# Optimization experiments

Hardware: AMD Instinct MI355X
Metric: run time of the kernel (lower is better)

## Reference

```python
import jax, jax.numpy as jnp
import numpy as np

B, A, N = 8, 512, 64           # structures, atoms, neighbors
D, F, G = 128, 128, 25         # atom basis, filters, gaussians
L = 3                          # interaction blocks
GA = 512                       # angular feature dim = 2*n_zetas*2*n_angular*n_zetas
MAXZ = 100
CUTOFF, START = 5.0, 1.2
LN2 = 0.6931471805599453


def ssp(x):
    # shifted softplus: ln(1+exp(x)) - ln(2)
    return jax.nn.softplus(x) - LN2


def setup_inputs() -> dict:
    key = jax.random.key(0)
    ks = jax.random.split(key, 16)
    atomic_numbers = jax.random.randint(ks[0], (B, A), 0, MAXZ, dtype=jnp.int32)
    positions = jax.random.normal(ks[1], (B, A, 3), dtype=jnp.float32) * 3.0
    neighbors = jax.random.randint(ks[2], (B, A, N), 0, A, dtype=jnp.int32)
    neighbor_mask = jax.random.randint(ks[3], (B, A, N), 0, 2, dtype=jnp.int32)
    G_i = jax.random.normal(ks[4], (B, A, GA), dtype=jnp.float32)
    s = 0.05
    embedding = jax.random.normal(ks[5], (MAXZ, D), dtype=jnp.float32) * 0.1
    embedding = embedding.at[0].set(0.0)  # padding_idx=0
    inp = {
        'atomic_numbers': atomic_numbers,
        'positions': positions,
        'neighbors': neighbors,
        'neighbor_mask': neighbor_mask,
        'G_i': G_i,
        'embedding': embedding,
        'filt_w1': jax.random.normal(ks[6], (L, G, F), dtype=jnp.float32) * s,
        'filt_b1': jnp.zeros((L, F), jnp.float32),
        'filt_w2': jax.random.normal(ks[7], (L, F, F), dtype=jnp.float32) * s,
        'filt_b2': jnp.zeros((L, F), jnp.float32),
        'in2f_w': jax.random.normal(ks[8], (L, D, F), dtype=jnp.float32) * s,
        'f2out_w': jax.random.normal(ks[9], (L, F, D), dtype=jnp.float32) * s,
        'f2out_b': jnp.zeros((L, D), jnp.float32),
        'dense_w': jax.random.normal(ks[10], (L, D, D), dtype=jnp.float32) * s,
        'dense_b': jnp.zeros((L, D), jnp.float32),
        'ang_w': jax.random.normal(ks[11], (L, GA, D), dtype=jnp.float32) * s,
    }
    return inp


def reference(atomic_numbers, positions, neighbors, neighbor_mask, G_i,
              embedding, filt_w1, filt_b1, filt_w2, filt_b2,
              in2f_w, f2out_w, f2out_b, dense_w, dense_b, ang_w):
    gather = jax.vmap(lambda feat, idx: feat[idx])  # per-structure neighbor gather

    x = embedding[atomic_numbers]                    # [B,A,D]

    # AtomDistances: gather neighbor positions and take pairwise norms
    pos_j = gather(positions, neighbors)             # [B,A,N,3]
    dvec = pos_j - positions[:, :, None, :]
    r_ij = jnp.sqrt(jnp.sum(dvec * dvec, axis=-1) + 1e-12)  # [B,A,N]

    # GaussianSmearing(start, cutoff, n_gaussians)
    offsets = jnp.linspace(START, CUTOFF, G).astype(x.dtype)
    width = offsets[1] - offsets[0]
    f_ij = jnp.exp((-0.5 / (width * width)) * (r_ij[..., None] - offsets) ** 2)  # [B,A,N,G]

    C = (r_ij <= CUTOFF).astype(x.dtype)             # HardCutoff [B,A,N]
    mask = neighbor_mask.astype(x.dtype)             # [B,A,N]

    for l in range(in2f_w.shape[0]):
        # filter-generating network on expanded distances, modulated by cutoff
        W = ssp(f_ij @ filt_w1[l] + filt_b1[l]) @ filt_w2[l] + filt_b2[l]  # [B,A,N,F]
        W = W * C[..., None]
        # CFConv: project, gather neighbors, filter-weight, masked neighbor sum
        y = x @ in2f_w[l]                            # [B,A,F]
        y_j = gather(y, neighbors)                   # [B,A,N,F]
        agg = jnp.sum(y_j * W * mask[..., None], axis=2)  # [B,A,F]
        v_rad = agg @ f2out_w[l] + f2out_b[l]        # f2out (activation=None)
        v_rad = v_rad @ dense_w[l] + dense_b[l]      # self.dense
        v_ang = G_i @ ang_w[l]                       # dense_angular (no bias)
        x = x + ssp(v_rad + v_ang)                   # residual interaction update
    return x
```

## Files before the change

kernel.cpp:

```cpp
#include <hip/hip_runtime.h>
#include <math.h>

#define NB 8
#define NA 512
#define NN 64
#define ND 128
#define NF 128
#define NG 25
#define NGA 512
#define TABN 1024

typedef __attribute__((ext_vector_type(8))) short bf16x8;
typedef __attribute__((ext_vector_type(4))) float f32x4;

__device__ __forceinline__ float sspf(float v) {
  return fmaxf(v, 0.0f) + __logf(1.0f + __expf(-fabsf(v))) - 0.6931471805599453f;
}

__device__ __forceinline__ short f2bf(float x) {
  union { float f; unsigned u; } v; v.f = x;
  unsigned r = v.u + 0x7fffu + ((v.u >> 16) & 1u);
  return (short)(r >> 16);
}

#if defined(__has_builtin)
#if __has_builtin(__builtin_amdgcn_cvt_pk_bf16_f32)
#define HAS_PKBF 1
#endif
#endif

__device__ __forceinline__ unsigned pk2bf(float a, float b) {
#ifdef HAS_PKBF
  typedef __attribute__((ext_vector_type(2))) __bf16 v2bf;
  union { v2bf v; unsigned u; } c;
  c.v = __builtin_amdgcn_cvt_pk_bf16_f32(a, b);
  return c.u;
#else
  union { float f; unsigned u; } x, y; x.f = a; y.f = b;
  const unsigned ra = (x.u + 0x7fffu + ((x.u >> 16) & 1u)) >> 16;
  const unsigned rb = (y.u + 0x7fffu + ((y.u >> 16) & 1u)) & 0xffff0000u;
  return ra | rb;
#endif
}

__device__ __forceinline__ float bf2f(unsigned short us) {
  union { unsigned u; float f; } v; v.u = ((unsigned)us) << 16; return v.f;
}

__device__ __forceinline__ bf16x8 pack8(float4 a, float4 b) {
  bf16x8 r;
  unsigned* p = (unsigned*)&r;
  p[0] = pk2bf(a.x, a.y); p[1] = pk2bf(a.z, a.w);
  p[2] = pk2bf(b.x, b.y); p[3] = pk2bf(b.z, b.w);
  return r;
}

__device__ __forceinline__ bf16x8 fragT(const float* __restrict__ M, int ldn,
                                        int n, int k0q) {
  float e[8];
#pragma unroll
  for (int i = 0; i < 8; ++i) e[i] = M[(size_t)(k0q + i) * ldn + n];
  bf16x8 r; unsigned* p = (unsigned*)&r;
  p[0] = pk2bf(e[0], e[1]); p[1] = pk2bf(e[2], e[3]);
  p[2] = pk2bf(e[4], e[5]); p[3] = pk2bf(e[6], e[7]);
  return r;
}

#define NW1 (3 * 128 * 32)
#define NSQ (3 * 128 * 128)
#define NAWT (3 * 128 * 512)

#define P1_TT 96
#define P1_AT (P1_TT + 192)
#define P1_W1 (P1_AT + 48)
#define P1_PF (P1_W1 + 24)
#define P1_TOT (P1_PF + 1024)

#define P2_VA 768
#define P2_Y0 (P2_VA + 256)
#define P2_TOT (P2_Y0 + 192)

__global__ __launch_bounds__(256) void k_prep1(
    const float* __restrict__ fw1, const float* __restrict__ fw2,
    const float* __restrict__ in2f, const float* __restrict__ aw,
    const float* __restrict__ f2o, const float* __restrict__ f2ob,
    const float* __restrict__ dw, const float* __restrict__ db,
    const float* __restrict__ Gi,
    short* __restrict__ w1T, short* __restrict__ w2T,
    short* __restrict__ in2fT, short* __restrict__ W12T,
    float* __restrict__ b12, short* __restrict__ awT,
    short* __restrict__ GiB) {
  __shared__ alignas(16) short sTile[32][33];
  const int bx = blockIdx.x;
  const int t = threadIdx.x;
  const int lane = t & 63, wave = t >> 6;
  const int lanelo = lane & 15, quad = lane >> 4;
  const int wbase = wave << 5;

  if (bx < P1_TT) {
    const int mat = bx >> 4, tile = bx & 15;
    const int l = mat >> 1, which = mat & 1;
    const float* src = (which ? in2f : fw2) + (size_t)l * 16384;
    short* dst = (which ? in2fT : w2T) + (size_t)l * 16384;
    const int tk0 = (tile >> 2) << 5, tn0 = (tile & 3) << 5;
    const int tr = t >> 3, tc4 = (t & 7) << 2;
    const float4 v = *(const float4*)(src + (size_t)(tk0 + tr) * 128 + tn0 + tc4);
    sTile[tr][tc4] = f2bf(v.x); sTile[tr][tc4 + 1] = f2bf(v.y);
    sTile[tr][tc4 + 2] = f2bf(v.z); sTile[tr][tc4 + 3] = f2bf(v.w);
    __syncthreads();
    short o[4];
#pragma unroll
    for (int j = 0; j < 4; ++j) o[j] = sTile[tc4 + j][tr];
    uint2 pk;
    pk.x = ((unsigned)(unsigned short)o[0]) | (((unsigned)(unsigned short)o[1]) << 16);
    pk.y = ((unsigned)(unsigned short)o[2]) | (((unsigned)(unsigned short)o[3]) << 16);
    *(uint2*)(dst + (size_t)(tn0 + tr) * 128 + tk0 + tc4) = pk;
    return;
  }
  if (bx < P1_AT) {
    const int ab = bx - P1_TT;
    const int l = ab >> 6, tile = ab & 63;
    const int tk0 = (tile >> 2) << 5, tn0 = (tile & 3) << 5;
    const float* src = aw + (size_t)l * 65536;
    short* dst = awT + (size_t)l * 65536;
    const int tr = t >> 3, tc4 = (t & 7) << 2;
    const float4 v = *(const float4*)(src + (size_t)(tk0 + tr) * 128 + tn0 + tc4);
    sTile[tr][tc4] = f2bf(v.x); sTile[tr][tc4 + 1] = f2bf(v.y);
    sTile[tr][tc4 + 2] = f2bf(v.z); sTile[tr][tc4 + 3] = f2bf(v.w);
    __syncthreads();
    short o[4];
#pragma unroll
    for (int j = 0; j < 4; ++j) o[j] = sTile[tc4 + j][tr];
    uint2 pk;
    pk.x = ((unsigned)(unsigned short)o[0]) | (((unsigned)(unsigned short)o[1]) << 16);
    pk.y = ((unsigned)(unsigned short)o[2]) | (((unsigned)(unsigned short)o[3]) << 16);
    *(uint2*)(dst + (size_t)(tn0 + tr) * 512 + tk0 + tc4) = pk;
    return;
  }
  if (bx < P1_W1) {
    const int idx = (bx - P1_AT) * 256 + t;
    const int l = idx >> 12, r = idx & 4095, n = r >> 5, k = r & 31;
    w1T[idx] = (k < NG) ? f2bf(fw1[(size_t)l * NG * NF + k * NF + n]) : (short)0;
    return;
  }
  if (bx < P1_PF) {
    const int fb = bx - P1_W1;
    const int l = fb >> 3, xi = fb & 7;
    const int i = (xi << 4) + lanelo;
    const float* f2o_l = f2o + (size_t)l * 16384;
    const float* dw_l = dw + (size_t)l * 16384;
    short* W12T_l = W12T + (size_t)l * 16384;
    f32x4 c[2] = {{0.f, 0.f, 0.f, 0.f}, {0.f, 0.f, 0.f, 0.f}};
#pragma unroll
    for (int kt = 0; kt < 4; ++kt) {
      const int k0 = kt * 32 + quad * 8;
      const bf16x8 b = pack8(*(const float4*)(f2o_l + (size_t)i * 128 + k0),
                             *(const float4*)(f2o_l + (size_t)i * 128 + k0 + 4));
#pragma unroll
      for (int ct = 0; ct < 2; ++ct) {
        const bf16x8 a = fragT(dw_l, 128, wbase + ct * 16 + lanelo, k0);
        c[ct] = __builtin_amdgcn_mfma_f32_16x16x32_bf16(a, b, c[ct], 0, 0, 0);
      }
    }
#pragma unroll
    for (int ct = 0; ct < 2; ++ct)
#pragma unroll
      for (int reg = 0; reg < 4; ++reg) {
        const int j = wbase + ct * 16 + quad * 4 + reg;
        W12T_l[(size_t)j * 128 + i] = f2bf(c[ct][reg]);
      }
    if (xi == 0 && t < 128) {
      float acc = db[(size_t)l * 128 + t];
      for (int k = 0; k < 128; ++k)
        acc += f2ob[(size_t)l * 128 + k] * dw_l[(size_t)k * 128 + t];
      b12[(size_t)l * 128 + t] = acc;
    }
    return;
  }
  {
    const int idx = ((bx - P1_PF) << 8) + t;
    const float* g = Gi + (size_t)idx * 8;
    const bf16x8 v = pack8(*(const float4*)g, *(const float4*)(g + 4));
    *(bf16x8*)(GiB + (size_t)idx * 8) = v;
  }
}

#define SHPAD 136
__global__ __launch_bounds__(256) void k_prep2(
    const float* __restrict__ emb, const int* __restrict__ zn,
    const short* __restrict__ GiB, const short* __restrict__ awT,
    const short* __restrict__ in2fT,
    const short* __restrict__ w1T, const short* __restrict__ w2T,
    const float* __restrict__ fb1, const float* __restrict__ fb2,
    short* __restrict__ vangB, float* __restrict__ x, short* __restrict__ yB,
    float* __restrict__ Ttab) {
  __shared__ alignas(16) short sH[16 * SHPAD];
  const int bx = blockIdx.x;
  const int t = threadIdx.x;
  const int lane = t & 63, wave = t >> 6;
  const int lanelo = lane & 15, quad = lane >> 4;
  const int wbase = wave << 5;

  if (bx < P2_VA) {
    const int l = bx >> 8;
    const int row = ((bx & 255) << 4) + lanelo;
    const short* awT_l = awT + (size_t)l * 65536;
    f32x4 c[2] = {{0.f, 0.f, 0.f, 0.f}, {0.f, 0.f, 0.f, 0.f}};
#pragma unroll
    for (int kt = 0; kt < 16; ++kt) {
      const int k0 = kt * 32 + quad * 8;
      const bf16x8 b = *(const bf16x8*)(GiB + (size_t)row * NGA + k0);
#pragma unroll
      for (int ct = 0; ct < 2; ++ct) {
        const bf16x8 a = *(const bf16x8*)(awT_l + (size_t)(wbase + ct * 16 + lanelo) * 512 + k0);
        c[ct] = __builtin_amdgcn_mfma_f32_16x16x32_bf16(a, b, c[ct], 0, 0, 0);
      }
    }
    short* vrow = vangB + ((size_t)l * NB * NA + row) * 128;
#pragma unroll
    for (int ct = 0; ct < 2; ++ct) {
      uint2 pk; pk.x = pk2bf(c[ct][0], c[ct][1]); pk.y = pk2bf(c[ct][2], c[ct][3]);
      *(uint2*)(vrow + wbase + ct * 16 + quad * 4) = pk;
    }
    return;
  }
  if (bx < P2_Y0) {
    const int row = ((bx - P2_VA) << 4) + lanelo;
    const float* erow = emb + (size_t)zn[row] * ND;
    f32x4 c[2] = {{0.f, 0.f, 0.f, 0.f}, {0.f, 0.f, 0.f, 0.f}};
#pragma unroll
    for (int kt = 0; kt < 4; ++kt) {
      const int k0 = kt * 32 + quad * 8;
      const float4 e0 = *(const float4*)(erow + k0);
      const float4 e1 = *(const float4*)(erow + k0 + 4);
      if (wave == 0) {
        *(float4*)(x + (size_t)row * ND + k0) = e0;
        *(float4*)(x + (size_t)row * ND + k0 + 4) = e1;
      }
      const bf16x8 b = pack8(e0, e1);
#pragma unroll
      for (int ct = 0; ct < 2; ++ct) {
        const bf16x8 a = *(const bf16x8*)(in2fT + (size_t)(wbase + ct * 16 + lanelo) * 128 + k0);
        c[ct] = __builtin_amdgcn_mfma_f32_16x16x32_bf16(a, b, c[ct], 0, 0, 0);
      }
    }
#pragma unroll
    for (int ct = 0; ct < 2; ++ct) {
      const int c0 = wbase + ct * 16 + quad * 4;
      uint2 pk; pk.x = pk2bf(c[ct][0], c[ct][1]); pk.y = pk2bf(c[ct][2], c[ct][3]);
      *(uint2*)(yB + (size_t)row * 128 + c0) = pk;
    }
    return;
  }
  {
    const int tb = bx - P2_Y0;
    const int l = tb >> 6;
    const int chunk = tb & 63;
    const short* w1Tl = w1T + (size_t)l * 128 * 32;
    const short* w2Tl = w2T + (size_t)l * 16384;
    const float* b1 = fb1 + (size_t)l * NF;
    const float* b2 = fb2 + (size_t)l * NF;

    bf16x8 bw1[2];
    bf16x8 bw2[8];
#pragma unroll
    for (int ct = 0; ct < 2; ++ct) {
      const int n = wbase + ct * 16 + lanelo;
      bw1[ct] = *(const bf16x8*)(w1Tl + n * 32 + quad * 8);
#pragma unroll
      for (int kt = 0; kt < 4; ++kt)
        bw2[ct * 4 + kt] = *(const bf16x8*)(w2Tl + n * 128 + kt * 32 + quad * 8);
    }
    float4 b1v[2];
    float b2r[2];
#pragma unroll
    for (int ct = 0; ct < 2; ++ct) {
      b1v[ct] = *(const float4*)(b1 + wbase + ct * 16 + quad * 4);
      b2r[ct] = b2[wbase + ct * 16 + lanelo];
    }

    const float stepg = 3.8f / 24.0f;
    const float coef = -0.5f / (stepg * stepg);
    const float rv = (float)(chunk * 16 + lanelo) * (5.0f / 1023.0f);
    bf16x8 gb;
    {
      float e[8];
#pragma unroll
      for (int i = 0; i < 8; ++i) {
        const int g = quad * 8 + i;
        const float d = rv - (1.2f + stepg * (float)g);
        e[i] = (g < NG) ? __expf(coef * d * d) : 0.0f;
      }
      unsigned* gp = (unsigned*)&gb;
      gp[0] = pk2bf(e[0], e[1]); gp[1] = pk2bf(e[2], e[3]);
      gp[2] = pk2bf(e[4], e[5]); gp[3] = pk2bf(e[6], e[7]);
    }
#pragma unroll
    for (int ct = 0; ct < 2; ++ct) {
      f32x4 c = {0.f, 0.f, 0.f, 0.f};
      c = __builtin_amdgcn_mfma_f32_16x16x32_bf16(bw1[ct], gb, c, 0, 0, 0);
      const int f0 = wbase + ct * 16 + quad * 4;
      uint2 pk;
      pk.x = pk2bf(sspf(c[0] + b1v[ct].x), sspf(c[1] + b1v[ct].y));
      pk.y = pk2bf(sspf(c[2] + b1v[ct].z), sspf(c[3] + b1v[ct].w));
      *(uint2*)(sH + lanelo * SHPAD + f0) = pk;
    }
    __syncthreads();
    f32x4 acc[2];
    acc[0] = (f32x4){b2r[0], b2r[0], b2r[0], b2r[0]};
    acc[1] = (f32x4){b2r[1], b2r[1], b2r[1], b2r[1]};
#pragma unroll
    for (int kt = 0; kt < 4; ++kt) {
      const bf16x8 ah = *(const bf16x8*)(sH + lanelo * SHPAD + kt * 32 + quad * 8);
#pragma unroll
      for (int ct = 0; ct < 2; ++ct)
        acc[ct] = __builtin_amdgcn_mfma_f32_16x16x32_bf16(ah, bw2[ct * 4 + kt], acc[ct], 0, 0, 0);
    }
#pragma unroll
    for (int ct = 0; ct < 2; ++ct)
#pragma unroll
      for (int reg = 0; reg < 4; ++reg) {
        const int rrow = chunk * 16 + quad * 4 + reg;
        const int f = wbase + ct * 16 + lanelo;
        Ttab[((size_t)l * TABN + rrow) * NF + f] = acc[ct][reg];
      }
  }
}

#define TPAD 136
#define APAD 136
__global__ __launch_bounds__(512) void k_layer(
    const float* __restrict__ pos, const int* __restrict__ nbr,
    const int* __restrict__ nmask, const short* __restrict__ yIn,
    const float* __restrict__ Tt,
    float* __restrict__ x, const short* __restrict__ vangL,
    const short* __restrict__ W12Tl, const float* __restrict__ b12l,
    const short* __restrict__ in2fTn, short* __restrict__ yOut) {
  __shared__ alignas(16) float2 sA[8][2][NN];
  __shared__ alignas(16) int2 sM[8][2][NN];
  __shared__ alignas(16) float sAgg[16][APAD];
  __shared__ alignas(16) short sT[16 * TPAD];

  const int t = threadIdx.x;
  const int lane = t & 63;
  const int wave = t >> 6;
  const int lanelo = lane & 15;
  const int quad = lane >> 4;
  const int ga0 = blockIdx.x << 4;
  const int b0 = ga0 & ~(NA - 1);

  int nvv[2];
#pragma unroll
  for (int aa = 0; aa < 2; ++aa) {
    const int al = (wave << 1) + aa;
    const int ga = ga0 + al;
    sA[wave][aa][lane] = make_float2(0.f, 0.f);
    sM[wave][aa][lane] = make_int2(0, b0 * NF);
    const int nj = nbr[(size_t)ga * NN + lane];
    const int mk = nmask[(size_t)ga * NN + lane];
    const float px = pos[(size_t)ga * 3];
    const float py = pos[(size_t)ga * 3 + 1];
    const float pz = pos[(size_t)ga * 3 + 2];
    const float* pj = pos + (size_t)(b0 + nj) * 3;
    const float dx = pj[0] - px, dy = pj[1] - py, dz = pj[2] - pz;
    const float r = sqrtf(dx * dx + dy * dy + dz * dz + 1e-12f);
    const bool valid = (r <= 5.0f) && (mk != 0);
    const unsigned long long m = __ballot(valid);
    const int posc = __popcll(m & ((1ull << lane) - 1ull));
    const float tt = r * ((float)(TABN - 1) / 5.0f);
    int k0 = (int)tt; if (k0 > TABN - 2) k0 = TABN - 2;
    const float fr = tt - (float)k0;
    if (valid) {
      sA[wave][aa][posc] = make_float2(1.0f - fr, fr);
      sM[wave][aa][posc] = make_int2(k0 * NF, (b0 + nj) * NF);
    }
    nvv[aa] = (int)__popcll(m);
  }

  const unsigned short* yu = (const unsigned short*)yIn;
#pragma unroll
  for (int aa = 0; aa < 2; ++aa) {
    float acc0 = 0.f, acc1 = 0.f;
    const int ntc = (nvv[aa] + 3) & ~3;
    for (int c = 0; c < ntc; c += 4) {
#pragma unroll
      for (int u = 0; u < 4; ++u) {
        const float2 w = sA[wave][aa][c + u];
        const int2 off = sM[wave][aa][c + u];
        const float t0a = Tt[off.x + lane];
        const float t0b = Tt[off.x + lane + 64];
        const float t1a = Tt[off.x + NF + lane];
        const float t1b = Tt[off.x + NF + lane + 64];
        const float wva = fmaf(w.x, t0a, w.y * t1a);
        const float wvb = fmaf(w.x, t0b, w.y * t1b);
        acc0 = fmaf(wva, bf2f(yu[off.y + lane]), acc0);
        acc1 = fmaf(wvb, bf2f(yu[off.y + lane + 64]), acc1);
      }
    }
    const int al = (wave << 1) + aa;
    sAgg[al][lane] = acc0;
    sAgg[al][lane + 64] = acc1;
  }
  __syncthreads();

  f32x4 c2 = {0.f, 0.f, 0.f, 0.f};
#pragma unroll
  for (int kt = 0; kt < 4; ++kt) {
    const float* ar = &sAgg[lanelo][kt * 32 + quad * 8];
    const bf16x8 b = pack8(*(const float4*)ar, *(const float4*)(ar + 4));
    const bf16x8 a = *(const bf16x8*)(W12Tl + ((wave << 4) + lanelo) * 128 + kt * 32 + quad * 8);
    c2 = __builtin_amdgcn_mfma_f32_16x16x32_bf16(a, b, c2, 0, 0, 0);
  }

  const int c0 = (wave << 4) + quad * 4;
  const int row = ga0 + lanelo;
  {
    const float4 dv = *(const float4*)(b12l + c0);
    const unsigned short* vp = (const unsigned short*)(vangL + (size_t)row * 128 + c0);
    float* xp = x + (size_t)row * 128 + c0;
    const float4 xv = *(const float4*)xp;
    float4 xo;
    xo.x = xv.x + sspf(c2[0] + bf2f(vp[0]) + dv.x);
    xo.y = xv.y + sspf(c2[1] + bf2f(vp[1]) + dv.y);
    xo.z = xv.z + sspf(c2[2] + bf2f(vp[2]) + dv.z);
    xo.w = xv.w + sspf(c2[3] + bf2f(vp[3]) + dv.w);
    *(float4*)xp = xo;
    if (in2fTn != nullptr) {
      uint2 pk; pk.x = pk2bf(xo.x, xo.y); pk.y = pk2bf(xo.z, xo.w);
      *(uint2*)(sT + lanelo * TPAD + c0) = pk;
    }
  }
  if (in2fTn == nullptr) return;
  __syncthreads();

  f32x4 c3 = {0.f, 0.f, 0.f, 0.f};
#pragma unroll
  for (int kt = 0; kt < 4; ++kt) {
    const bf16x8 b = *(const bf16x8*)(sT + lanelo * TPAD + kt * 32 + quad * 8);
    const bf16x8 a = *(const bf16x8*)(in2fTn + ((wave << 4) + lanelo) * 128 + kt * 32 + quad * 8);
    c3 = __builtin_amdgcn_mfma_f32_16x16x32_bf16(a, b, c3, 0, 0, 0);
  }
  uint2 pk; pk.x = pk2bf(c3[0], c3[1]); pk.y = pk2bf(c3[2], c3[3]);
  *(uint2*)(yOut + (size_t)row * 128 + c0) = pk;
}

extern "C" void kernel_launch(void* const* d_in, const int* in_sizes, int n_in,
                              void* d_out, int out_size, void* d_ws, size_t ws_size,
                              hipStream_t stream) {
  (void)in_sizes; (void)n_in; (void)out_size; (void)ws_size;
  const int* zn = (const int*)d_in[0];
  const float* pos = (const float*)d_in[1];
  const int* nbr = (const int*)d_in[2];
  const int* nmask = (const int*)d_in[3];
  const float* Gi = (const float*)d_in[4];
  const float* emb = (const float*)d_in[5];
  const float* fw1 = (const float*)d_in[6];
  const float* fb1 = (const float*)d_in[7];
  const float* fw2 = (const float*)d_in[8];
  const float* fb2 = (const float*)d_in[9];
  const float* in2f = (const float*)d_in[10];
  const float* f2o = (const float*)d_in[11];
  const float* f2ob = (const float*)d_in[12];
  const float* dwp = (const float*)d_in[13];
  const float* dbp = (const float*)d_in[14];
  const float* awp = (const float*)d_in[15];

  float* x = (float*)d_out;
  float* b12 = (float*)d_ws;
  float* Ttab = b12 + 3 * 128;
  short* vangB = (short*)(Ttab + (size_t)3 * TABN * NF);
  short* yA = vangB + (size_t)3 * NB * NA * ND;
  short* yBb = yA + (size_t)NB * NA * NF;
  short* in2fT = yBb + (size_t)NB * NA * NF;
  short* W12T = in2fT + NSQ;
  short* awT = W12T + NSQ;
  short* GiB = awT + NAWT;
  short* w1T = GiB + (size_t)NB * NA * NGA;
  short* w2T = w1T + NW1;

  k_prep1<<<P1_TOT, 256, 0, stream>>>(
      fw1, fw2, in2f, awp, f2o, f2ob, dwp, dbp, Gi,
      w1T, w2T, in2fT, W12T, b12, awT, GiB);
  k_prep2<<<P2_TOT, 256, 0, stream>>>(
      emb, zn, GiB, awT, in2fT, w1T, w2T, fb1, fb2,
      vangB, x, yA, Ttab);

  short* yin = yA;
  short* yout = yBb;
  for (int l = 0; l < 3; ++l) {
    k_layer<<<NB * NA / 16, 512, 0, stream>>>(pos, nbr, nmask, yin,
        Ttab + (size_t)l * TABN * NF,
        x, vangB + (size_t)l * NB * NA * ND,
        W12T + (size_t)l * 16384, b12 + (size_t)l * 128,
        (l < 2) ? (in2fT + (size_t)(l + 1) * 16384) : nullptr, yout);
    short* tmp = yin; yin = yout; yout = tmp;
  }
}
```

Measured before the change: 149.7 us.

## Precompute compacted neighbor entries once and rebalance prep and layer kernels

Neighbor compaction (distance, table index, interpolation weights, gather offset) moves into the first prep kernel and is written once to a workspace that all three layer launches reuse, instead of being recomputed per layer. The filter table build moves from the second prep kernel into the first, reading fp32 weights directly rather than staged bf16 copies. The Gi bf16 staging pass is dropped and Gi is converted on the fly. Layer blocks now handle 8 atoms, one per wave, which doubles the grid, but half of each MFMA tile in the dense epilogue is wasted.

```diff
diff --git a/kernel.cpp b/kernel.cpp
--- a/kernel.cpp
+++ b/kernel.cpp
@@ -66,43 +66,62 @@
   return r;
 }
 
-#define NW1 (3 * 128 * 32)
-#define NSQ (3 * 128 * 128)
-#define NAWT (3 * 128 * 512)
-
-#define P1_TT 96
-#define P1_AT (P1_TT + 192)
-#define P1_W1 (P1_AT + 48)
-#define P1_PF (P1_W1 + 24)
-#define P1_TOT (P1_PF + 1024)
+__device__ __forceinline__ bf16x8 fragT25(const float* __restrict__ M,
+                                          int n, int k0q) {
+  float e[8];
+#pragma unroll
+  for (int i = 0; i < 8; ++i)
+    e[i] = (k0q + i < NG) ? M[(size_t)(k0q + i) * NF + n] : 0.0f;
+  bf16x8 r; unsigned* p = (unsigned*)&r;
+  p[0] = pk2bf(e[0], e[1]); p[1] = pk2bf(e[2], e[3]);
+  p[2] = pk2bf(e[4], e[5]); p[3] = pk2bf(e[6], e[7]);
+  return r;
+}
+
+#define B_TT 48
+#define B_AT (B_TT + 192)
+#define B_PF (B_AT + 24)
+#define B_TAB (B_PF + 192)
+#define P1_TOT (B_TAB + 1024)
 
 #define P2_VA 768
-#define P2_Y0 (P2_VA + 256)
-#define P2_TOT (P2_Y0 + 192)
+#define P2_TOT (P2_VA + 256)
 
 __global__ __launch_bounds__(256) void k_prep1(
-    const float* __restrict__ fw1, const float* __restrict__ fw2,
+    const float* __restrict__ fw1, const float* __restrict__ fb1,
+    const float* __restrict__ fw2, const float* __restrict__ fb2,
     const float* __restrict__ in2f, const float* __restrict__ aw,
     const float* __restrict__ f2o, const float* __restrict__ f2ob,
     const float* __restrict__ dw, const float* __restrict__ db,
-    const float* __restrict__ Gi,
-    short* __restrict__ w1T, short* __restrict__ w2T,
-    short* __restrict__ in2fT, short* __restrict__ W12T,
-    float* __restrict__ b12, short* __restrict__ awT,
-    short* __restrict__ GiB) {
+    const float* __restrict__ pos, const int* __restrict__ nbr,
+    const int* __restrict__ nmask,
+    short* __restrict__ in2fT, short* __restrict__ awT,
+    short* __restrict__ W12T, float* __restrict__ b12,
+    float* __restrict__ Ttab, int4* __restrict__ ent,
+    int* __restrict__ nvArr) {
   __shared__ alignas(16) short sTile[32][33];
+  __shared__ alignas(16) short sH[16 * 136];
+  __shared__ alignas(16) int4 sCmp[4][NN];
   const int bx = blockIdx.x;
   const int t = threadIdx.x;
   const int lane = t & 63, wave = t >> 6;
   const int lanelo = lane & 15, quad = lane >> 4;
   const int wbase = wave << 5;
 
-  if (bx < P1_TT) {
-    const int mat = bx >> 4, tile = bx & 15;
-    const int l = mat >> 1, which = mat & 1;
-    const float* src = (which ? in2f : fw2) + (size_t)l * 16384;
-    short* dst = (which ? in2fT : w2T) + (size_t)l * 16384;
-    const int tk0 = (tile >> 2) << 5, tn0 = (tile & 3) << 5;
+  if (bx < B_AT) {
+    const float* src; short* dst; int tk0, tn0, stride;
+    if (bx < B_TT) {
+      const int l = bx >> 4, tile = bx & 15;
+      src = in2f + (size_t)l * 16384;
+      dst = in2fT + (size_t)l * 16384;
+      tk0 = (tile >> 2) << 5; tn0 = (tile & 3) << 5; stride = 128;
+    } else {
+      const int ab = bx - B_TT;
+      const int l = ab >> 6, tile = ab & 63;
+      src = aw + (size_t)l * 65536;
+      dst = awT + (size_t)l * 65536;
+      tk0 = (tile >> 2) << 5; tn0 = (tile & 3) << 5; stride = 512;
+    }
     const int tr = t >> 3, tc4 = (t & 7) << 2;
     const float4 v = *(const float4*)(src + (size_t)(tk0 + tr) * 128 + tn0 + tc4);
     sTile[tr][tc4] = f2bf(v.x); sTile[tr][tc4 + 1] = f2bf(v.y);
@@ -114,37 +133,11 @@
     uint2 pk;
     pk.x = ((unsigned)(unsigned short)o[0]) | (((unsigned)(unsigned short)o[1]) << 16);
     pk.y = ((unsigned)(unsigned short)o[2]) | (((unsigned)(unsigned short)o[3]) << 16);
-    *(uint2*)(dst + (size_t)(tn0 + tr) * 128 + tk0 + tc4) = pk;
+    *(uint2*)(dst + (size_t)(tn0 + tr) * stride + tk0 + tc4) = pk;
     return;
   }
-  if (bx < P1_AT) {
-    const int ab = bx - P1_TT;
-    const int l = ab >> 6, tile = ab & 63;
-    const int tk0 = (tile >> 2) << 5, tn0 = (tile & 3) << 5;
-    const float* src = aw + (size_t)l * 65536;
-    short* dst = awT + (size_t)l * 65536;
-    const int tr = t >> 3, tc4 = (t & 7) << 2;
-    const float4 v = *(const float4*)(src + (size_t)(tk0 + tr) * 128 + tn0 + tc4);
-    sTile[tr][tc4] = f2bf(v.x); sTile[tr][tc4 + 1] = f2bf(v.y);
-    sTile[tr][tc4 + 2] = f2bf(v.z); sTile[tr][tc4 + 3] = f2bf(v.w);
-    __syncthreads();
-    short o[4];
-#pragma unroll
-    for (int j = 0; j < 4; ++j) o[j] = sTile[tc4 + j][tr];
-    uint2 pk;
-    pk.x = ((unsigned)(unsigned short)o[0]) | (((unsigned)(unsigned short)o[1]) << 16);
-    pk.y = ((unsigned)(unsigned short)o[2]) | (((unsigned)(unsigned short)o[3]) << 16);
-    *(uint2*)(dst + (size_t)(tn0 + tr) * 512 + tk0 + tc4) = pk;
-    return;
-  }
-  if (bx < P1_W1) {
-    const int idx = (bx - P1_AT) * 256 + t;
-    const int l = idx >> 12, r = idx & 4095, n = r >> 5, k = r & 31;
-    w1T[idx] = (k < NG) ? f2bf(fw1[(size_t)l * NG * NF + k * NF + n]) : (short)0;
-    return;
-  }
-  if (bx < P1_PF) {
-    const int fb = bx - P1_W1;
+  if (bx < B_PF) {
+    const int fb = bx - B_AT;
     const int l = fb >> 3, xi = fb & 7;
     const int i = (xi << 4) + lanelo;
     const float* f2o_l = f2o + (size_t)l * 16384;
@@ -177,100 +170,15 @@
     }
     return;
   }
-  {
-    const int idx = ((bx - P1_PF) << 8) + t;
-    const float* g = Gi + (size_t)idx * 8;
-    const bf16x8 v = pack8(*(const float4*)g, *(const float4*)(g + 4));
-    *(bf16x8*)(GiB + (size_t)idx * 8) = v;
-  }
-}
-
-#define SHPAD 136
-__global__ __launch_bounds__(256) void k_prep2(
-    const float* __restrict__ emb, const int* __restrict__ zn,
-    const short* __restrict__ GiB, const short* __restrict__ awT,
-    const short* __restrict__ in2fT,
-    const short* __restrict__ w1T, const short* __restrict__ w2T,
-    const float* __restrict__ fb1, const float* __restrict__ fb2,
-    short* __restrict__ vangB, float* __restrict__ x, short* __restrict__ yB,
-    float* __restrict__ Ttab) {
-  __shared__ alignas(16) short sH[16 * SHPAD];
-  const int bx = blockIdx.x;
-  const int t = threadIdx.x;
-  const int lane = t & 63, wave = t >> 6;
-  const int lanelo = lane & 15, quad = lane >> 4;
-  const int wbase = wave << 5;
-
-  if (bx < P2_VA) {
-    const int l = bx >> 8;
-    const int row = ((bx & 255) << 4) + lanelo;
-    const short* awT_l = awT + (size_t)l * 65536;
-    f32x4 c[2] = {{0.f, 0.f, 0.f, 0.f}, {0.f, 0.f, 0.f, 0.f}};
-#pragma unroll
-    for (int kt = 0; kt < 16; ++kt) {
-      const int k0 = kt * 32 + quad * 8;
-      const bf16x8 b = *(const bf16x8*)(GiB + (size_t)row * NGA + k0);
-#pragma unroll
-      for (int ct = 0; ct < 2; ++ct) {
-        const bf16x8 a = *(const bf16x8*)(awT_l + (size_t)(wbase + ct * 16 + lanelo) * 512 + k0);
-        c[ct] = __builtin_amdgcn_mfma_f32_16x16x32_bf16(a, b, c[ct], 0, 0, 0);
-      }
-    }
-    short* vrow = vangB + ((size_t)l * NB * NA + row) * 128;
-#pragma unroll
-    for (int ct = 0; ct < 2; ++ct) {
-      uint2 pk; pk.x = pk2bf(c[ct][0], c[ct][1]); pk.y = pk2bf(c[ct][2], c[ct][3]);
-      *(uint2*)(vrow + wbase + ct * 16 + quad * 4) = pk;
-    }
-    return;
-  }
-  if (bx < P2_Y0) {
-    const int row = ((bx - P2_VA) << 4) + lanelo;
-    const float* erow = emb + (size_t)zn[row] * ND;
-    f32x4 c[2] = {{0.f, 0.f, 0.f, 0.f}, {0.f, 0.f, 0.f, 0.f}};
-#pragma unroll
-    for (int kt = 0; kt < 4; ++kt) {
-      const int k0 = kt * 32 + quad * 8;
-      const float4 e0 = *(const float4*)(erow + k0);
-      const float4 e1 = *(const float4*)(erow + k0 + 4);
-      if (wave == 0) {
-        *(float4*)(x + (size_t)row * ND + k0) = e0;
-        *(float4*)(x + (size_t)row * ND + k0 + 4) = e1;
-      }
-      const bf16x8 b = pack8(e0, e1);
-#pragma unroll
-      for (int ct = 0; ct < 2; ++ct) {
-        const bf16x8 a = *(const bf16x8*)(in2fT + (size_t)(wbase + ct * 16 + lanelo) * 128 + k0);
-        c[ct] = __builtin_amdgcn_mfma_f32_16x16x32_bf16(a, b, c[ct], 0, 0, 0);
-      }
-    }
-#pragma unroll
-    for (int ct = 0; ct < 2; ++ct) {
-      const int c0 = wbase + ct * 16 + quad * 4;
-      uint2 pk; pk.x = pk2bf(c[ct][0], c[ct][1]); pk.y = pk2bf(c[ct][2], c[ct][3]);
-      *(uint2*)(yB + (size_t)row * 128 + c0) = pk;
-    }
-    return;
-  }
-  {
-    const int tb = bx - P2_Y0;
+  if (bx < B_TAB) {
+    const int tb = bx - B_PF;
     const int l = tb >> 6;
     const int chunk = tb & 63;
-    const short* w1Tl = w1T + (size_t)l * 128 * 32;
-    const short* w2Tl = w2T + (size_t)l * 16384;
+    const float* fw1_l = fw1 + (size_t)l * NG * NF;
+    const float* fw2_l = fw2 + (size_t)l * 16384;
     const float* b1 = fb1 + (size_t)l * NF;
     const float* b2 = fb2 + (size_t)l * NF;
 
-    bf16x8 bw1[2];
-    bf16x8 bw2[8];
-#pragma unroll
-    for (int ct = 0; ct < 2; ++ct) {
-      const int n = wbase + ct * 16 + lanelo;
-      bw1[ct] = *(const bf16x8*)(w1Tl + n * 32 + quad * 8);
-#pragma unroll
-      for (int kt = 0; kt < 4; ++kt)
-        bw2[ct * 4 + kt] = *(const bf16x8*)(w2Tl + n * 128 + kt * 32 + quad * 8);
-    }
     float4 b1v[2];
     float b2r[2];
 #pragma unroll
@@ -297,13 +205,14 @@
     }
 #pragma unroll
     for (int ct = 0; ct < 2; ++ct) {
+      const bf16x8 a = fragT25(fw1_l, wbase + ct * 16 + lanelo, quad * 8);
       f32x4 c = {0.f, 0.f, 0.f, 0.f};
-      c = __builtin_amdgcn_mfma_f32_16x16x32_bf16(bw1[ct], gb, c, 0, 0, 0);
+      c = __builtin_amdgcn_mfma_f32_16x16x32_bf16(a, gb, c, 0, 0, 0);
       const int f0 = wbase + ct * 16 + quad * 4;
       uint2 pk;
       pk.x = pk2bf(sspf(c[0] + b1v[ct].x), sspf(c[1] + b1v[ct].y));
       pk.y = pk2bf(sspf(c[2] + b1v[ct].z), sspf(c[3] + b1v[ct].w));
-      *(uint2*)(sH + lanelo * SHPAD + f0) = pk;
+      *(uint2*)(sH + lanelo * 136 + f0) = pk;
     }
     __syncthreads();
     f32x4 acc[2];
@@ -311,10 +220,12 @@
     acc[1] = (f32x4){b2r[1], b2r[1], b2r[1], b2r[1]};
 #pragma unroll
     for (int kt = 0; kt < 4; ++kt) {
-      const bf16x8 ah = *(const bf16x8*)(sH + lanelo * SHPAD + kt * 32 + quad * 8);
-#pragma unroll
-      for (int ct = 0; ct < 2; ++ct)
-        acc[ct] = __builtin_amdgcn_mfma_f32_16x16x32_bf16(ah, bw2[ct * 4 + kt], acc[ct], 0, 0, 0);
+      const bf16x8 ah = *(const bf16x8*)(sH + lanelo * 136 + kt * 32 + quad * 8);
+#pragma unroll
+      for (int ct = 0; ct < 2; ++ct) {
+        const bf16x8 a = fragT(fw2_l, 128, wbase + ct * 16 + lanelo, kt * 32 + quad * 8);
+        acc[ct] = __builtin_amdgcn_mfma_f32_16x16x32_bf16(ah, a, acc[ct], 0, 0, 0);
+      }
     }
 #pragma unroll
     for (int ct = 0; ct < 2; ++ct)
@@ -324,38 +235,11 @@
         const int f = wbase + ct * 16 + lanelo;
         Ttab[((size_t)l * TABN + rrow) * NF + f] = acc[ct][reg];
       }
-  }
-}
-
-#define TPAD 136
-#define APAD 136
-__global__ __launch_bounds__(512) void k_layer(
-    const float* __restrict__ pos, const int* __restrict__ nbr,
-    const int* __restrict__ nmask, const short* __restrict__ yIn,
-    const float* __restrict__ Tt,
-    float* __restrict__ x, const short* __restrict__ vangL,
-    const short* __restrict__ W12Tl, const float* __restrict__ b12l,
-    const short* __restrict__ in2fTn, short* __restrict__ yOut) {
-  __shared__ alignas(16) float2 sA[8][2][NN];
-  __shared__ alignas(16) int2 sM[8][2][NN];
-  __shared__ alignas(16) float sAgg[16][APAD];
-  __shared__ alignas(16) short sT[16 * TPAD];
-
-  const int t = threadIdx.x;
-  const int lane = t & 63;
-  const int wave = t >> 6;
-  const int lanelo = lane & 15;
-  const int quad = lane >> 4;
-  const int ga0 = blockIdx.x << 4;
-  const int b0 = ga0 & ~(NA - 1);
-
-  int nvv[2];
-#pragma unroll
-  for (int aa = 0; aa < 2; ++aa) {
-    const int al = (wave << 1) + aa;
-    const int ga = ga0 + al;
-    sA[wave][aa][lane] = make_float2(0.f, 0.f);
-    sM[wave][aa][lane] = make_int2(0, b0 * NF);
+    return;
+  }
+  {
+    const int ga = (bx - B_TAB) * 4 + wave;
+    const int b0 = ga & ~(NA - 1);
     const int nj = nbr[(size_t)ga * NN + lane];
     const int mk = nmask[(size_t)ga * NN + lane];
     const float px = pos[(size_t)ga * 3];
@@ -370,37 +254,120 @@
     const float tt = r * ((float)(TABN - 1) / 5.0f);
     int k0 = (int)tt; if (k0 > TABN - 2) k0 = TABN - 2;
     const float fr = tt - (float)k0;
-    if (valid) {
-      sA[wave][aa][posc] = make_float2(1.0f - fr, fr);
-      sM[wave][aa][posc] = make_int2(k0 * NF, (b0 + nj) * NF);
-    }
-    nvv[aa] = (int)__popcll(m);
-  }
+    sCmp[wave][lane] = make_int4(0, b0 * NF, 0, 0);
+    if (valid)
+      sCmp[wave][posc] = make_int4(k0 * NF, (b0 + nj) * NF,
+                                   __float_as_int(1.0f - fr), __float_as_int(fr));
+    ent[(size_t)ga * NN + lane] = sCmp[wave][lane];
+    if (lane == 0) nvArr[ga] = (int)__popcll(m);
+  }
+}
+
+__global__ __launch_bounds__(256) void k_prep2(
+    const float* __restrict__ emb, const int* __restrict__ zn,
+    const float* __restrict__ Gi, const short* __restrict__ awT,
+    const short* __restrict__ in2fT,
+    short* __restrict__ vangB, float* __restrict__ x, short* __restrict__ yB) {
+  const int bx = blockIdx.x;
+  const int t = threadIdx.x;
+  const int lane = t & 63, wave = t >> 6;
+  const int lanelo = lane & 15, quad = lane >> 4;
+  const int wbase = wave << 5;
+
+  if (bx < P2_VA) {
+    const int l = bx >> 8;
+    const int row = ((bx & 255) << 4) + lanelo;
+    const short* awT_l = awT + (size_t)l * 65536;
+    const float* grow = Gi + (size_t)row * NGA;
+    f32x4 c[2] = {{0.f, 0.f, 0.f, 0.f}, {0.f, 0.f, 0.f, 0.f}};
+#pragma unroll
+    for (int kt = 0; kt < 16; ++kt) {
+      const int k0 = kt * 32 + quad * 8;
+      const bf16x8 b = pack8(*(const float4*)(grow + k0),
+                             *(const float4*)(grow + k0 + 4));
+#pragma unroll
+      for (int ct = 0; ct < 2; ++ct) {
+        const bf16x8 a = *(const bf16x8*)(awT_l + (size_t)(wbase + ct * 16 + lanelo) * 512 + k0);
+        c[ct] = __builtin_amdgcn_mfma_f32_16x16x32_bf16(a, b, c[ct], 0, 0, 0);
+      }
+    }
+    short* vrow = vangB + ((size_t)l * NB * NA + row) * 128;
+#pragma unroll
+    for (int ct = 0; ct < 2; ++ct) {
+      uint2 pk; pk.x = pk2bf(c[ct][0], c[ct][1]); pk.y = pk2bf(c[ct][2], c[ct][3]);
+      *(uint2*)(vrow + wbase + ct * 16 + quad * 4) = pk;
+    }
+    return;
+  }
+  {
+    const int row = ((bx - P2_VA) << 4) + lanelo;
+    const float* erow = emb + (size_t)zn[row] * ND;
+    f32x4 c[2] = {{0.f, 0.f, 0.f, 0.f}, {0.f, 0.f, 0.f, 0.f}};
+#pragma unroll
+    for (int kt = 0; kt < 4; ++kt) {
+      const int k0 = kt * 32 + quad * 8;
+      const float4 e0 = *(const float4*)(erow + k0);
+      const float4 e1 = *(const float4*)(erow + k0 + 4);
+      if (wave == 0) {
+        *(float4*)(x + (size_t)row * ND + k0) = e0;
+        *(float4*)(x + (size_t)row * ND + k0 + 4) = e1;
+      }
+      const bf16x8 b = pack8(e0, e1);
+#pragma unroll
+      for (int ct = 0; ct < 2; ++ct) {
+        const bf16x8 a = *(const bf16x8*)(in2fT + (size_t)(wbase + ct * 16 + lanelo) * 128 + k0);
+        c[ct] = __builtin_amdgcn_mfma_f32_16x16x32_bf16(a, b, c[ct], 0, 0, 0);
+      }
+    }
+#pragma unroll
+    for (int ct = 0; ct < 2; ++ct) {
+      const int c0 = wbase + ct * 16 + quad * 4;
+      uint2 pk; pk.x = pk2bf(c[ct][0], c[ct][1]); pk.y = pk2bf(c[ct][2], c[ct][3]);
+      *(uint2*)(yB + (size_t)row * 128 + c0) = pk;
+    }
+  }
+}
+
+__global__ __launch_bounds__(512) void k_layer(
+    const short* __restrict__ yIn, const float* __restrict__ Tt,
+    float* __restrict__ x, const short* __restrict__ vangL,
+    const short* __restrict__ W12Tl, const float* __restrict__ b12l,
+    const short* __restrict__ in2fTn, short* __restrict__ yOut,
+    const int4* __restrict__ ent, const int* __restrict__ nvArr) {
+  __shared__ alignas(16) int4 sEnt[8][NN];
+  __shared__ alignas(16) float sAgg[16][136];
+  __shared__ alignas(16) short sT[16 * 136];
+
+  const int t = threadIdx.x;
+  const int lane = t & 63;
+  const int wave = t >> 6;
+  const int lanelo = lane & 15;
+  const int quad = lane >> 4;
+  const int ga0 = blockIdx.x << 3;
+
+  sEnt[wave][lane] = ent[(size_t)(ga0 + wave) * NN + lane];
+  const int nv = nvArr[ga0 + wave];
 
   const unsigned short* yu = (const unsigned short*)yIn;
-#pragma unroll
-  for (int aa = 0; aa < 2; ++aa) {
-    float acc0 = 0.f, acc1 = 0.f;
-    const int ntc = (nvv[aa] + 3) & ~3;
-    for (int c = 0; c < ntc; c += 4) {
-#pragma unroll
-      for (int u = 0; u < 4; ++u) {
-        const float2 w = sA[wave][aa][c + u];
-        const int2 off = sM[wave][aa][c + u];
-        const float t0a = Tt[off.x + lane];
-        const float t0b = Tt[off.x + lane + 64];
-        const float t1a = Tt[off.x + NF + lane];
-        const float t1b = Tt[off.x + NF + lane + 64];
-        const float wva = fmaf(w.x, t0a, w.y * t1a);
-        const float wvb = fmaf(w.x, t0b, w.y * t1b);
-        acc0 = fmaf(wva, bf2f(yu[off.y + lane]), acc0);
-        acc1 = fmaf(wvb, bf2f(yu[off.y + lane + 64]), acc1);
-      }
-    }
-    const int al = (wave << 1) + aa;
-    sAgg[al][lane] = acc0;
-    sAgg[al][lane + 64] = acc1;
-  }
+  float acc0 = 0.f, acc1 = 0.f;
+  const int ntc = (nv + 3) & ~3;
+  for (int c = 0; c < ntc; c += 4) {
+#pragma unroll
+    for (int u = 0; u < 4; ++u) {
+      const int4 e = sEnt[wave][c + u];
+      const float w0 = __int_as_float(e.z), w1 = __int_as_float(e.w);
+      const float t0a = Tt[e.x + lane];
+      const float t0b = Tt[e.x + lane + 64];
+      const float t1a = Tt[e.x + NF + lane];
+      const float t1b = Tt[e.x + NF + lane + 64];
+      const float wva = fmaf(w0, t0a, w1 * t1a);
+      const float wvb = fmaf(w0, t0b, w1 * t1b);
+      acc0 = fmaf(wva, bf2f(yu[e.y + lane]), acc0);
+      acc1 = fmaf(wvb, bf2f(yu[e.y + lane + 64]), acc1);
+    }
+  }
+  sAgg[wave][lane] = acc0;
+  sAgg[wave][lane + 64] = acc1;
   __syncthreads();
 
   f32x4 c2 = {0.f, 0.f, 0.f, 0.f};
@@ -414,7 +381,7 @@
 
   const int c0 = (wave << 4) + quad * 4;
   const int row = ga0 + lanelo;
-  {
+  if (lanelo < 8) {
     const float4 dv = *(const float4*)(b12l + c0);
     const unsigned short* vp = (const unsigned short*)(vangL + (size_t)row * 128 + c0);
     float* xp = x + (size_t)row * 128 + c0;
@@ -427,7 +394,7 @@
     *(float4*)xp = xo;
     if (in2fTn != nullptr) {
       uint2 pk; pk.x = pk2bf(xo.x, xo.y); pk.y = pk2bf(xo.z, xo.w);
-      *(uint2*)(sT + lanelo * TPAD + c0) = pk;
+      *(uint2*)(sT + lanelo * 136 + c0) = pk;
     }
   }
   if (in2fTn == nullptr) return;
@@ -436,12 +403,14 @@
   f32x4 c3 = {0.f, 0.f, 0.f, 0.f};
 #pragma unroll
   for (int kt = 0; kt < 4; ++kt) {
-    const bf16x8 b = *(const bf16x8*)(sT + lanelo * TPAD + kt * 32 + quad * 8);
+    const bf16x8 b = *(const bf16x8*)(sT + lanelo * 136 + kt * 32 + quad * 8);
     const bf16x8 a = *(const bf16x8*)(in2fTn + ((wave << 4) + lanelo) * 128 + kt * 32 + quad * 8);
     c3 = __builtin_amdgcn_mfma_f32_16x16x32_bf16(a, b, c3, 0, 0, 0);
   }
-  uint2 pk; pk.x = pk2bf(c3[0], c3[1]); pk.y = pk2bf(c3[2], c3[3]);
-  *(uint2*)(yOut + (size_t)row * 128 + c0) = pk;
+  if (lanelo < 8) {
+    uint2 pk; pk.x = pk2bf(c3[0], c3[1]); pk.y = pk2bf(c3[2], c3[3]);
+    *(uint2*)(yOut + (size_t)row * 128 + c0) = pk;
+  }
 }
 
 extern "C" void kernel_launch(void* const* d_in, const int* in_sizes, int n_in,
@@ -472,27 +441,27 @@
   short* yA = vangB + (size_t)3 * NB * NA * ND;
   short* yBb = yA + (size_t)NB * NA * NF;
   short* in2fT = yBb + (size_t)NB * NA * NF;
-  short* W12T = in2fT + NSQ;
-  short* awT = W12T + NSQ;
-  short* GiB = awT + NAWT;
-  short* w1T = GiB + (size_t)NB * NA * NGA;
-  short* w2T = w1T + NW1;
+  short* W12T = in2fT + (size_t)3 * 128 * 128;
+  short* awT = W12T + (size_t)3 * 128 * 128;
+  int4* ent = (int4*)(awT + (size_t)3 * 128 * 512);
+  int* nvArr = (int*)(ent + (size_t)NB * NA * NN);
 
   k_prep1<<<P1_TOT, 256, 0, stream>>>(
-      fw1, fw2, in2f, awp, f2o, f2ob, dwp, dbp, Gi,
-      w1T, w2T, in2fT, W12T, b12, awT, GiB);
+      fw1, fb1, fw2, fb2, in2f, awp, f2o, f2ob, dwp, dbp,
+      pos, nbr, nmask,
+      in2fT, awT, W12T, b12, Ttab, ent, nvArr);
   k_prep2<<<P2_TOT, 256, 0, stream>>>(
-      emb, zn, GiB, awT, in2fT, w1T, w2T, fb1, fb2,
-      vangB, x, yA, Ttab);
+      emb, zn, Gi, awT, in2fT, vangB, x, yA);
 
   short* yin = yA;
   short* yout = yBb;
   for (int l = 0; l < 3; ++l) {
-    k_layer<<<NB * NA / 16, 512, 0, stream>>>(pos, nbr, nmask, yin,
+    k_layer<<<NB * NA / 8, 512, 0, stream>>>(yin,
         Ttab + (size_t)l * TABN * NF,
         x, vangB + (size_t)l * NB * NA * ND,
         W12T + (size_t)l * 16384, b12 + (size_t)l * 128,
-        (l < 2) ? (in2fT + (size_t)(l + 1) * 16384) : nullptr, yout);
+        (l < 2) ? (in2fT + (size_t)(l + 1) * 16384) : nullptr, yout,
+        ent, nvArr);
     short* tmp = yin; yin = yout; yout = tmp;
   }
 }
```

Measured after the change: 149.7 us. About the same (-0.1%).
